# Optimization experiments

Hardware: AMD Instinct MI355X
Metric: run time of the kernel (lower is better)

The kernel has to match this reference:

```python
import jax, jax.numpy as jnp
import numpy as np

B, C, H, W = 16, 512, 25, 25
HEADS = 8
HID = 2048
PATCH = 5  # hardcoded patch_size in FusionAttention
EPS_LN = 1e-5
EPS_BN = 1e-5


def _channel_layernorm(x, g, b):
    # torch: std = var(unbiased=False).sqrt(); (x-mean)/(std+eps)*g + b, over channel dim=1
    mean = jnp.mean(x, axis=1, keepdims=True)
    var = jnp.var(x, axis=1, keepdims=True)
    return (x - mean) / (jnp.sqrt(var) + EPS_LN) * g + b


def _dwconv3x3(x, w, b):
    # depthwise 3x3, padding 1; w: (C,1,3,3)
    y = jax.lax.conv_general_dilated(
        x, w, window_strides=(1, 1), padding=((1, 1), (1, 1)),
        feature_group_count=x.shape[1],
        dimension_numbers=('NCHW', 'OIHW', 'NCHW'))
    return y + b[None, :, None, None]


def setup_inputs() -> dict:
    key = jax.random.key(0)
    ks = jax.random.split(key, 20)
    s = 0.02
    d = {
        'x': jax.random.normal(ks[0], (B, C, H, W), jnp.float32),
        'ln1_g': jnp.ones((1, C, 1, 1), jnp.float32),
        'ln1_b': jnp.zeros((1, C, 1, 1), jnp.float32),
        'wq': jax.random.normal(ks[1], (C, 1, 3, 3), jnp.float32) * s,
        'bq': jnp.zeros((C,), jnp.float32),
        'wk': jax.random.normal(ks[2], (C, 1, 3, 3), jnp.float32) * s,
        'bk': jnp.zeros((C,), jnp.float32),
        'wv': jax.random.normal(ks[3], (C, 1, 3, 3), jnp.float32) * s,
        'bv': jnp.zeros((C,), jnp.float32),
        'swq': jax.random.normal(ks[4], (C, 1, 3, 3), jnp.float32) * s,
        'sbq': jnp.zeros((C,), jnp.float32),
        'swk': jax.random.normal(ks[5], (C, 1, 3, 3), jnp.float32) * s,
        'sbk': jnp.zeros((C,), jnp.float32),
        'swv': jax.random.normal(ks[6], (C, 1, 3, 3), jnp.float32) * s,
        'sbv': jnp.zeros((C,), jnp.float32),
        'proj_w': jax.random.normal(ks[7], (C, C, 1, 1), jnp.float32) * s,
        'bn_g': jnp.ones((C,), jnp.float32),
        'bn_b': jnp.zeros((C,), jnp.float32),
        'bn_mean': jnp.zeros((C,), jnp.float32),
        'bn_var': jnp.ones((C,), jnp.float32),
        'ln2_g': jnp.ones((1, C, 1, 1), jnp.float32),
        'ln2_b': jnp.zeros((1, C, 1, 1), jnp.float32),
        'w1': jax.random.normal(ks[8], (HID, C, 1, 1), jnp.float32) * s,
        'b1': jnp.zeros((HID,), jnp.float32),
        'w2': jax.random.normal(ks[9], (C, HID, 1, 1), jnp.float32) * s,
        'b2': jnp.zeros((C,), jnp.float32),
    }
    return d


def _fusion_attention(x, wq, bq, wk, bk, wv, bv, swq, sbq, swk, sbk, swv, sbv,
                      proj_w, bn_g, bn_b, bn_mean, bn_var):
    b, c, h, w = x.shape
    n = h * w
    hd = c // HEADS
    scale = hd ** -0.5

    def split_heads(t):  # (b,c,h,w) -> (b, heads, n, hd)
        return t.reshape(b, HEADS, hd, n).transpose(0, 1, 3, 2)

    q = split_heads(_dwconv3x3(x, wq, bq))
    k = split_heads(_dwconv3x3(x, wk, bk))
    v = split_heads(_dwconv3x3(x, wv, bv))

    dots = jnp.einsum('bhid,bhjd->bhij', q, k) * scale
    attn = jax.nn.softmax(dots, axis=-1)
    out = jnp.einsum('bhij,bhjd->bhid', attn, v)
    # rearrange 'b h (H W) d -> b (h d) H W' with H=PATCH
    out = out.transpose(0, 1, 3, 2).reshape(b, c, PATCH, n // PATCH)

    spe_q = _dwconv3x3(out, swq, sbq).reshape(b, c, n)          # b d (l w)
    spe_k = _dwconv3x3(out, swk, sbk).reshape(b, c, n).transpose(0, 2, 1)  # b (l w) d
    spe_v = _dwconv3x3(out, swv, sbv).reshape(b, c, n)

    attention = jax.nn.softmax(jnp.einsum('bcn,bnd->bcd', spe_q, spe_k) * scale, axis=-1)
    x_out = jnp.einsum('bcd,bdn->bcn', attention, spe_v).reshape(b, c, h, w)

    # 1x1 conv (no bias) + BatchNorm2d (eval mode)
    proj = jnp.einsum('oc,bchw->bohw', proj_w[:, :, 0, 0], x_out)
    proj = (proj - bn_mean[None, :, None, None]) / jnp.sqrt(bn_var + EPS_BN)[None, :, None, None]
    proj = proj * bn_g[None, :, None, None] + bn_b[None, :, None, None]
    return proj


def _feedforward(x, w1, b1, w2, b2):
    h1 = jnp.einsum('oc,bchw->bohw', w1[:, :, 0, 0], x) + b1[None, :, None, None]
    h1 = jax.nn.gelu(h1, approximate=False)
    return jnp.einsum('oc,bchw->bohw', w2[:, :, 0, 0], h1) + b2[None, :, None, None]


def reference(x, ln1_g, ln1_b, wq, bq, wk, bk, wv, bv, swq, sbq, swk, sbk,
              swv, sbv, proj_w, bn_g, bn_b, bn_mean, bn_var, ln2_g, ln2_b,
              w1, b1, w2, b2):
    y1 = x + _fusion_attention(_channel_layernorm(x, ln1_g, ln1_b),
                               wq, bq, wk, bk, wv, bv, swq, sbq, swk, sbk,
                               swv, sbv, proj_w, bn_g, bn_b, bn_mean, bn_var)
    y_out = y1 + _feedforward(_channel_layernorm(y1, ln2_g, ln2_b), w1, b1, w2, b2)
    return y_out
```

## Files before the change

kernel.cpp:

```cpp
#include <hip/hip_runtime.h>
#include <math.h>

constexpr int BATCH = 16;
constexpr int CH    = 512;
constexpr int NPIX  = 625;
constexpr int HEADS = 8;
constexpr int HDIM  = 64;
constexpr int HIDD  = 2048;

constexpr float EPS_LN = 1e-5f;
constexpr float EPS_BN = 1e-5f;
constexpr float SCALE  = 0.125f;

typedef __bf16 bf16x8 __attribute__((ext_vector_type(8)));
typedef float  f32x4  __attribute__((ext_vector_type(4)));

static __device__ inline unsigned pack_bf16(float lo, float hi) {
  union { __bf16 h; unsigned short u; } a, b;
  a.h = (__bf16)lo; b.h = (__bf16)hi;
  return ((unsigned)b.u << 16) | (unsigned)a.u;
}

__global__ __launch_bounds__(256) void ln_kernel2(
    const float* __restrict__ x, const float* __restrict__ g,
    const float* __restrict__ bt, float* __restrict__ y) {
  __shared__ float ps[4][64];
  __shared__ float pss[4][64];
  int lane = threadIdx.x & 63;
  int w    = threadIdx.x >> 6;
  int b    = blockIdx.y;
  int i    = blockIdx.x * 64 + lane;
  int ic   = i < NPIX ? i : NPIX - 1;
  const float* xb = x + (size_t)b * CH * NPIX + ic;
  float s = 0.f, ss = 0.f;
  #pragma unroll 4
  for (int c = w * 128; c < w * 128 + 128; ++c) {
    float v = xb[(size_t)c * NPIX];
    s += v; ss += v * v;
  }
  ps[w][lane] = s; pss[w][lane] = ss;
  __syncthreads();
  float st  = ps[0][lane] + ps[1][lane] + ps[2][lane] + ps[3][lane];
  float sst = pss[0][lane] + pss[1][lane] + pss[2][lane] + pss[3][lane];
  float mean = st * (1.0f / CH);
  float var  = sst * (1.0f / CH) - mean * mean;
  float inv  = 1.0f / (sqrtf(fmaxf(var, 0.0f)) + EPS_LN);
  if (i >= NPIX) return;
  float* yb = y + (size_t)b * CH * NPIX + i;
  #pragma unroll 4
  for (int c = w * 128; c < w * 128 + 128; ++c) {
    float v = xb[(size_t)c * NPIX];
    yb[(size_t)c * NPIX] = (v - mean) * inv * g[c] + bt[c];
  }
}

__global__ void dwconv3_kernel(const float* __restrict__ src,
    const float* __restrict__ w0, const float* __restrict__ b0,
    const float* __restrict__ w1, const float* __restrict__ b1,
    const float* __restrict__ w2, const float* __restrict__ b2,
    float* __restrict__ d0, float* __restrict__ d1, float* __restrict__ d2,
    int Hc, int Wc) {
  size_t idx = (size_t)blockIdx.x * blockDim.x + threadIdx.x;
  size_t total = (size_t)BATCH * CH * Hc * Wc;
  if (idx >= total) return;
  int wp = (int)(idx % Wc);
  int hp = (int)((idx / Wc) % Hc);
  int c  = (int)((idx / ((size_t)Wc * Hc)) % CH);
  const float* f0 = w0 + c * 9;
  const float* f1 = w1 + c * 9;
  const float* f2 = w2 + c * 9;
  float a0 = 0.f, a1 = 0.f, a2 = 0.f;
  #pragma unroll
  for (int kh = -1; kh <= 1; ++kh) {
    int h2 = hp + kh; if (h2 < 0 || h2 >= Hc) continue;
    #pragma unroll
    for (int kw = -1; kw <= 1; ++kw) {
      int w2p = wp + kw; if (w2p < 0 || w2p >= Wc) continue;
      float v = src[idx + (size_t)kh * Wc + kw];
      int wi = (kh + 1) * 3 + (kw + 1);
      a0 += v * f0[wi]; a1 += v * f1[wi]; a2 += v * f2[wi];
    }
  }
  d0[idx] = a0 + b0[c];
  d1[idx] = a1 + b1[c];
  d2[idx] = a2 + b2[c];
}

__global__ void dwconv_spe_kernel(const float* __restrict__ src,
    const float* __restrict__ w0, const float* __restrict__ b0,
    const float* __restrict__ w1, const float* __restrict__ b1,
    const float* __restrict__ w2, const float* __restrict__ b2,
    __bf16* __restrict__ q16, __bf16* __restrict__ k16, float* __restrict__ v) {
  size_t idx = (size_t)blockIdx.x * blockDim.x + threadIdx.x;
  if (idx >= (size_t)BATCH * CH * 640) return;
  int n = (int)(idx % 640);
  int c = (int)((idx / 640) % CH);
  int b = (int)(idx / ((size_t)640 * CH));
  if (n >= NPIX) { q16[idx] = (__bf16)0.f; k16[idx] = (__bf16)0.f; return; }
  int hp = n / 125, wp = n % 125;
  size_t base = ((size_t)b * CH + c) * NPIX;
  const float* f0 = w0 + c * 9;
  const float* f1 = w1 + c * 9;
  const float* f2 = w2 + c * 9;
  float a0 = 0.f, a1 = 0.f, a2 = 0.f;
  #pragma unroll
  for (int kh = -1; kh <= 1; ++kh) {
    int h2 = hp + kh; if (h2 < 0 || h2 >= 5) continue;
    #pragma unroll
    for (int kw = -1; kw <= 1; ++kw) {
      int w2p = wp + kw; if (w2p < 0 || w2p >= 125) continue;
      float vv = src[base + h2 * 125 + w2p];
      int wi = (kh + 1) * 3 + (kw + 1);
      a0 += vv * f0[wi]; a1 += vv * f1[wi]; a2 += vv * f2[wi];
    }
  }
  q16[idx] = (__bf16)(a0 + b0[c]);
  k16[idx] = (__bf16)(a1 + b1[c]);
  v[base + n] = a2 + b2[c];
}

__global__ __launch_bounds__(256) void qk_to_bf16T(
    const float* __restrict__ q, const float* __restrict__ k,
    __bf16* __restrict__ qT, __bf16* __restrict__ kT) {
  __shared__ __bf16 tq[64][65];
  __shared__ __bf16 tk[64][65];
  int bh = blockIdx.y;
  int n0 = blockIdx.x * 64;
  int b = bh >> 3, h = bh & 7;
  const float* qb = q + (size_t)(b * CH + h * HDIM) * NPIX;
  const float* kb = k + (size_t)(b * CH + h * HDIM) * NPIX;
  #pragma unroll
  for (int it = 0; it < 16; ++it) {
    int idx = threadIdx.x + it * 256;
    int d = idx >> 6, n = idx & 63;
    int nn = n0 + n;
    float qv = (nn < NPIX) ? qb[(size_t)d * NPIX + nn] : 0.f;
    float kv = (nn < NPIX) ? kb[(size_t)d * NPIX + nn] : 0.f;
    tq[n][d] = (__bf16)qv;
    tk[n][d] = (__bf16)kv;
  }
  __syncthreads();
  size_t obase = (size_t)bh * NPIX;
  #pragma unroll
  for (int it = 0; it < 16; ++it) {
    int idx = threadIdx.x + it * 256;
    int n = idx >> 6, d = idx & 63;
    int nn = n0 + n;
    if (nn < NPIX) {
      qT[(obase + nn) * 64 + d] = tq[n][d];
      kT[(obase + nn) * 64 + d] = tk[n][d];
    }
  }
}

__global__ void v_to_bf16(const float* __restrict__ v, __bf16* __restrict__ v16) {
  int row = blockIdx.x;
  const float* src = v + (size_t)row * NPIX;
  __bf16* dst = v16 + (size_t)row * 640;
  for (int n = threadIdx.x; n < NPIX; n += 256) dst[n] = (__bf16)src[n];
}

__global__ __launch_bounds__(256) void head_attn_mfma4(
    const __bf16* __restrict__ qT, const __bf16* __restrict__ kT,
    const __bf16* __restrict__ vB, float* __restrict__ out) {
  __shared__ __align__(16) union SmU {
    unsigned char p[16 * 1296];
    float ostage[64][17];
  } sm;
  __shared__ float red_max[4][16];
  __shared__ float red_sum[4][16];

  int t = threadIdx.x;
  int w = t >> 6, lane = t & 63, g = lane >> 4, li = lane & 15;
  int h = blockIdx.y, b = blockIdx.z;
  int bh = b * HEADS + h;
  int i0 = blockIdx.x * 16;
  const __bf16* Qb = qT + (size_t)bh * NPIX * 64;
  const __bf16* Kb = kT + (size_t)bh * NPIX * 64;

  bf16x8 aq0, aq1;
  {
    int qr = i0 + li; if (qr > NPIX - 1) qr = NPIX - 1;
    const __bf16* qp = Qb + (size_t)qr * 64 + 8 * g;
    aq0 = *(const bf16x8*)(qp);
    aq1 = *(const bf16x8*)(qp + 32);
  }

  f32x4 s[10];
  #pragma unroll
  for (int cfl = 0; cfl < 10; ++cfl) {
    int kc = (w * 10 + cfl) * 16 + li;
    int kcl = kc > NPIX - 1 ? NPIX - 1 : kc;
    const __bf16* kp = Kb + (size_t)kcl * 64 + 8 * g;
    bf16x8 bk0 = *(const bf16x8*)(kp);
    bf16x8 bk1 = *(const bf16x8*)(kp + 32);
    f32x4 a = (f32x4){0.f, 0.f, 0.f, 0.f};
    a = __builtin_amdgcn_mfma_f32_16x16x32_bf16(aq0, bk0, a, 0, 0, 0);
    a = __builtin_amdgcn_mfma_f32_16x16x32_bf16(aq1, bk1, a, 0, 0, 0);
    s[cfl] = a * SCALE;
  }
  if (w == 3 && li > 0) {
    s[9][0] = -1e30f; s[9][1] = -1e30f; s[9][2] = -1e30f; s[9][3] = -1e30f;
  }

  #pragma unroll
  for (int r = 0; r < 4; ++r) {
    float mx = s[0][r];
    #pragma unroll
    for (int cfl = 1; cfl < 10; ++cfl) mx = fmaxf(mx, s[cfl][r]);
    mx = fmaxf(mx, __shfl_xor(mx, 1));
    mx = fmaxf(mx, __shfl_xor(mx, 2));
    mx = fmaxf(mx, __shfl_xor(mx, 4));
    mx = fmaxf(mx, __shfl_xor(mx, 8));
    if (li == 0) red_max[w][4 * g + r] = mx;
  }
  __syncthreads();

  #pragma unroll
  for (int r = 0; r < 4; ++r) {
    int row = 4 * g + r;
    float mx = fmaxf(fmaxf(red_max[0][row], red_max[1][row]),
                     fmaxf(red_max[2][row], red_max[3][row]));
    float sum = 0.f;
    #pragma unroll
    for (int cfl = 0; cfl < 10; ++cfl) {
      float p = __expf(s[cfl][r] - mx);
      s[cfl][r] = p;
      sum += p;
    }
    sum += __shfl_xor(sum, 1);
    sum += __shfl_xor(sum, 2);
    sum += __shfl_xor(sum, 4);
    sum += __shfl_xor(sum, 8);
    if (li == 0) red_sum[w][row] = sum;
  }
  __syncthreads();

  #pragma unroll
  for (int cfp = 0; cfp < 5; ++cfp) {
    int cf0 = 2 * cfp, cf1 = cf0 + 1;
    #pragma unroll
    for (int r = 0; r < 4; ++r) {
      float v0 = s[cf0][r], v1 = s[cf1][r];
      float t0 = __shfl_xor(v0, 1);
      float t1 = __shfl_xor(v1, 1);
      bool even = (li & 1) == 0;
      float lo = even ? v0 : t1;
      float hi = even ? t0 : v1;
      int col = even ? ((w * 10 + cf0) * 16 + li)
                     : ((w * 10 + cf1) * 16 + li - 1);
      int row = 4 * g + r;
      *(unsigned*)(&sm.p[row * 1296 + col * 2]) = pack_bf16(lo, hi);
    }
  }
  __syncthreads();

  const __bf16* vrow = vB + (size_t)(b * CH + h * HDIM + w * 16 + li) * 640;
  f32x4 oa = (f32x4){0.f, 0.f, 0.f, 0.f};
  f32x4 ob = (f32x4){0.f, 0.f, 0.f, 0.f};
  #pragma unroll
  for (int ks = 0; ks < 20; ks += 2) {
    bf16x8 pa0 = *(const bf16x8*)(&sm.p[li * 1296 + ks * 64 + 16 * g]);
    bf16x8 bv0 = *(const bf16x8*)(vrow + ks * 32 + 8 * g);
    oa = __builtin_amdgcn_mfma_f32_16x16x32_bf16(pa0, bv0, oa, 0, 0, 0);
    bf16x8 pa1 = *(const bf16x8*)(&sm.p[li * 1296 + (ks + 1) * 64 + 16 * g]);
    bf16x8 bv1 = *(const bf16x8*)(vrow + (ks + 1) * 32 + 8 * g);
    ob = __builtin_amdgcn_mfma_f32_16x16x32_bf16(pa1, bv1, ob, 0, 0, 0);
  }
  f32x4 o = oa + ob;
  #pragma unroll
  for (int r = 0; r < 4; ++r) {
    int row = 4 * g + r;
    float l = red_sum[0][row] + red_sum[1][row] + red_sum[2][row] + red_sum[3][row];
    o[r] *= (1.0f / l);
  }
  __syncthreads();

  #pragma unroll
  for (int r = 0; r < 4; ++r)
    sm.ostage[w * 16 + li][4 * g + r] = o[r];
  __syncthreads();
  size_t cbase = (size_t)(b * CH + h * HDIM);
  #pragma unroll
  for (int it = 0; it < 4; ++it) {
    int e = t + it * 256;
    int d = e >> 4, nl = e & 15;
    int n = i0 + nl;
    if (n < NPIX) out[(cbase + d) * NPIX + n] = sm.ostage[d][nl];
  }
}

__global__ __launch_bounds__(256) void chan_attn_mfma2(
    const __bf16* __restrict__ sq, const __bf16* __restrict__ sk,
    __bf16* __restrict__ Am) {
  __shared__ float red_max[4][16];
  __shared__ float red_sum[4][16];
  int t = threadIdx.x;
  int w = t >> 6, lane = t & 63, g = lane >> 4, li = lane & 15;
  int b = blockIdx.y;
  int cq0 = blockIdx.x * 16;
  const __bf16* qrow  = sq + ((size_t)b * CH + cq0 + li) * 640 + 8 * g;
  const __bf16* kbase = sk + ((size_t)b * CH + w * 128 + li) * 640 + 8 * g;
  f32x4 acc[8];
  #pragma unroll
  for (int i = 0; i < 8; ++i) acc[i] = (f32x4){0.f, 0.f, 0.f, 0.f};
  for (int ks = 0; ks < 20; ++ks) {
    bf16x8 af = *(const bf16x8*)(qrow + ks * 32);
    #pragma unroll
    for (int cfl = 0; cfl < 8; ++cfl) {
      bf16x8 bfr = *(const bf16x8*)(kbase + (size_t)cfl * 16 * 640 + ks * 32);
      acc[cfl] = __builtin_amdgcn_mfma_f32_16x16x32_bf16(af, bfr, acc[cfl], 0, 0, 0);
    }
  }
  #pragma unroll
  for (int i = 0; i < 8; ++i) acc[i] = acc[i] * SCALE;

  #pragma unroll
  for (int r = 0; r < 4; ++r) {
    float mx = acc[0][r];
    #pragma unroll
    for (int cfl = 1; cfl < 8; ++cfl) mx = fmaxf(mx, acc[cfl][r]);
    mx = fmaxf(mx, __shfl_xor(mx, 1));
    mx = fmaxf(mx, __shfl_xor(mx, 2));
    mx = fmaxf(mx, __shfl_xor(mx, 4));
    mx = fmaxf(mx, __shfl_xor(mx, 8));
    if (li == 0) red_max[w][4 * g + r] = mx;
  }
  __syncthreads();

  #pragma unroll
  for (int r = 0; r < 4; ++r) {
    int row = 4 * g + r;
    float mx = fmaxf(fmaxf(red_max[0][row], red_max[1][row]),
                     fmaxf(red_max[2][row], red_max[3][row]));
    float sum = 0.f;
    #pragma unroll
    for (int cfl = 0; cfl < 8; ++cfl) {
      float p = __expf(acc[cfl][r] - mx);
      acc[cfl][r] = p;
      sum += p;
    }
    sum += __shfl_xor(sum, 1);
    sum += __shfl_xor(sum, 2);
    sum += __shfl_xor(sum, 4);
    sum += __shfl_xor(sum, 8);
    if (li == 0) red_sum[w][row] = sum;
  }
  __syncthreads();

  __bf16* Ab = Am + ((size_t)b * CH + cq0) * CH + w * 128;
  #pragma unroll
  for (int r = 0; r < 4; ++r) {
    int row = 4 * g + r;
    float l = red_sum[0][row] + red_sum[1][row] + red_sum[2][row] + red_sum[3][row];
    float inv = 1.0f / l;
    #pragma unroll
    for (int cfl = 0; cfl < 8; ++cfl)
      Ab[(size_t)row * CH + cfl * 16 + li] = (__bf16)(acc[cfl][r] * inv);
  }
}

template <int EPI>
__global__ __launch_bounds__(256) void gemm_nt(
    const __bf16* __restrict__ A, long long aBatch,
    const __bf16* __restrict__ B, long long bBatch,
    void* __restrict__ Cout, long long cBatch,
    int M, int N, int K,
    const float* __restrict__ p0, const float* __restrict__ p1,
    const float* __restrict__ res, long long resBatch) {
  __shared__ __align__(16) union {
    struct { unsigned char As[128 * 128]; unsigned char Bs[64 * 128]; } s;
    float Ce[4][64][17];
  } u;
  int t = threadIdx.x;
  int w = t >> 6, lane = t & 63, g = lane >> 4, li = lane & 15;
  int wm = w & 1, wn = w >> 1;
  int n0 = blockIdx.x * 64, m0 = blockIdx.y * 128, b = blockIdx.z;
  const __bf16* Ab = A + (size_t)b * aBatch;
  const __bf16* Bb = B + (size_t)b * bBatch;
  f32x4 acc[4][2];
  #pragma unroll
  for (int i = 0; i < 4; ++i)
    #pragma unroll
    for (int j = 0; j < 2; ++j) acc[i][j] = (f32x4){0.f, 0.f, 0.f, 0.f};

  for (int k0 = 0; k0 < K; k0 += 64) {
    bf16x8 ra[4], rb[2];
    #pragma unroll
    for (int i = 0; i < 4; ++i) {
      int e = t + i * 256;
      int row = e >> 3, cc = e & 7;
      int ar = m0 + row; ar = ar < M ? ar : M - 1;
      ra[i] = *(const bf16x8*)(Ab + (size_t)ar * K + k0 + cc * 8);
    }
    #pragma unroll
    for (int i = 0; i < 2; ++i) {
      int e = t + i * 256;
      int row = e >> 3, cc = e & 7;
      rb[i] = *(const bf16x8*)(Bb + (size_t)(n0 + row) * K + k0 + cc * 8);
    }
    __syncthreads();
    #pragma unroll
    for (int i = 0; i < 4; ++i) {
      int e = t + i * 256; int row = e >> 3, cc = e & 7;
      int off = (row * 128 + cc * 16) ^ ((row & 7) << 4);
      *(bf16x8*)(&u.s.As[off]) = ra[i];
    }
    #pragma unroll
    for (int i = 0; i < 2; ++i) {
      int e = t + i * 256; int row = e >> 3, cc = e & 7;
      int off = (row * 128 + cc * 16) ^ ((row & 7) << 4);
      *(bf16x8*)(&u.s.Bs[off]) = rb[i];
    }
    __syncthreads();
    #pragma unroll
    for (int ks = 0; ks < 2; ++ks) {
      bf16x8 af[4], bfr[2];
      #pragma unroll
      for (int mf = 0; mf < 4; ++mf) {
        int row = wm * 64 + mf * 16 + li;
        int off = (row * 128 + ks * 64 + g * 16) ^ ((row & 7) << 4);
        af[mf] = *(const bf16x8*)(&u.s.As[off]);
      }
      #pragma unroll
      for (int nf = 0; nf < 2; ++nf) {
        int row = wn * 32 + nf * 16 + li;
        int off = (row * 128 + ks * 64 + g * 16) ^ ((row & 7) << 4);
        bfr[nf] = *(const bf16x8*)(&u.s.Bs[off]);
      }
      #pragma unroll
      for (int mf = 0; mf < 4; ++mf)
        #pragma unroll
        for (int nf = 0; nf < 2; ++nf)
          acc[mf][nf] = __builtin_amdgcn_mfma_f32_16x16x32_bf16(
              af[mf], bfr[nf], acc[mf][nf], 0, 0, 0);
    }
    __syncthreads();
  }

  #pragma unroll
  for (int p = 0; p < 2; ++p) {
    __syncthreads();
    #pragma unroll
    for (int mf = 0; mf < 4; ++mf) {
      #pragma unroll
      for (int r = 0; r < 4; ++r)
        u.Ce[w][mf * 16 + 4 * g + r][li] = acc[mf][p][r];
    }
    __syncthreads();
    int m = m0 + wm * 64 + lane;
    int colb = n0 + wn * 32 + p * 16;
    if (m < M) {
      float vv[16];
      #pragma unroll
      for (int c = 0; c < 16; ++c) vv[c] = u.Ce[w][lane][c];
      if (EPI == 0) {
        __bf16* Cb = (__bf16*)Cout + (size_t)b * cBatch + (size_t)m * N + colb;
        bf16x8 o0, o1;
        #pragma unroll
        for (int j = 0; j < 8; ++j) { o0[j] = (__bf16)vv[j]; o1[j] = (__bf16)vv[8 + j]; }
        *(bf16x8*)(Cb) = o0;
        *(bf16x8*)(Cb + 8) = o1;
      } else if (EPI == 1) {
        float* Cf = (float*)Cout + (size_t)b * cBatch + (size_t)m * N + colb;
        const float* rp = res + (size_t)b * resBatch + (size_t)m * N + colb;
        #pragma unroll
        for (int c = 0; c < 16; ++c)
          vv[c] = vv[c] * p0[colb + c] + p1[colb + c] + rp[c];
        #pragma unroll
        for (int c4 = 0; c4 < 4; ++c4)
          *(f32x4*)(Cf + c4 * 4) = (f32x4){vv[c4*4], vv[c4*4+1], vv[c4*4+2], vv[c4*4+3]};
      } else if (EPI == 2) {
        __bf16* Cb = (__bf16*)Cout + (size_t)b * cBatch + (size_t)m * N + colb;
        #pragma unroll
        for (int c = 0; c < 16; ++c) {
          float xg = vv[c] + p0[colb + c];
          vv[c] = 0.5f * xg * (1.0f + erff(xg * 0.70710678118654752f));
        }
        bf16x8 o0, o1;
        #pragma unroll
        for (int j = 0; j < 8; ++j) { o0[j] = (__bf16)vv[j]; o1[j] = (__bf16)vv[8 + j]; }
        *(bf16x8*)(Cb) = o0;
        *(bf16x8*)(Cb + 8) = o1;
      } else {
        float* Cf = (float*)Cout + (size_t)b * cBatch + (size_t)m * N + colb;
        const float* rp = res + (size_t)b * resBatch + (size_t)m * N + colb;
        #pragma unroll
        for (int c = 0; c < 16; ++c)
          vv[c] = vv[c] + p0[colb + c] + rp[c];
        #pragma unroll
        for (int c4 = 0; c4 < 4; ++c4)
          *(f32x4*)(Cf + c4 * 4) = (f32x4){vv[c4*4], vv[c4*4+1], vv[c4*4+2], vv[c4*4+3]};
      }
    }
  }
}

template <typename TO>
__global__ __launch_bounds__(256) void transpose_bat(
    const float* __restrict__ in, TO* __restrict__ out, int R, int Cc) {
  __shared__ float tile[64][65];
  int b = blockIdx.z;
  int c0 = blockIdx.x * 64, r0 = blockIdx.y * 64;
  const float* ib = in + (size_t)b * R * Cc;
  TO* ob = out + (size_t)b * R * Cc;
  for (int e = threadIdx.x; e < 4096; e += 256) {
    int rr = e >> 6, cc = e & 63;
    int r = r0 + rr, c = c0 + cc;
    tile[rr][cc] = (r < R && c < Cc) ? ib[(size_t)r * Cc + c] : 0.f;
  }
  __syncthreads();
  for (int e = threadIdx.x; e < 4096; e += 256) {
    int cc = e >> 6, rr = e & 63;
    int r = r0 + rr, c = c0 + cc;
    if (r < R && c < Cc) ob[(size_t)c * R + r] = (TO)tile[rr][cc];
  }
}

__global__ __launch_bounds__(256) void ln2_row_kernel(
    const float* __restrict__ y, const float* __restrict__ g,
    const float* __restrict__ bt, __bf16* __restrict__ o) {
  int row = blockIdx.x * 4 + (threadIdx.x >> 6);
  int lane = threadIdx.x & 63;
  const float* yr = y + (size_t)row * CH + lane * 8;
  f32x4 v0 = *(const f32x4*)(yr);
  f32x4 v1 = *(const f32x4*)(yr + 4);
  float s = v0[0]+v0[1]+v0[2]+v0[3]+v1[0]+v1[1]+v1[2]+v1[3];
  float ss = v0[0]*v0[0]+v0[1]*v0[1]+v0[2]*v0[2]+v0[3]*v0[3]
           + v1[0]*v1[0]+v1[1]*v1[1]+v1[2]*v1[2]+v1[3]*v1[3];
  #pragma unroll
  for (int off = 32; off > 0; off >>= 1) {
    s  += __shfl_xor(s, off);
    ss += __shfl_xor(ss, off);
  }
  float mean = s * (1.0f / CH);
  float var  = ss * (1.0f / CH) - mean * mean;
  float inv  = 1.0f / (sqrtf(fmaxf(var, 0.0f)) + EPS_LN);
  f32x4 g0 = *(const f32x4*)(g + lane * 8);
  f32x4 g1 = *(const f32x4*)(g + lane * 8 + 4);
  f32x4 b0 = *(const f32x4*)(bt + lane * 8);
  f32x4 b1 = *(const f32x4*)(bt + lane * 8 + 4);
  bf16x8 ov;
  #pragma unroll
  for (int j = 0; j < 4; ++j) ov[j]     = (__bf16)((v0[j] - mean) * inv * g0[j] + b0[j]);
  #pragma unroll
  for (int j = 0; j < 4; ++j) ov[4 + j] = (__bf16)((v1[j] - mean) * inv * g1[j] + b1[j]);
  *(bf16x8*)(o + (size_t)row * CH + lane * 8) = ov;
}

__global__ void cast_bf16_kernel(const float* __restrict__ s, __bf16* __restrict__ d, int n) {
  int i = blockIdx.x * 256 + threadIdx.x;
  if (i < n) d[i] = (__bf16)s[i];
}

__global__ void bn_prep(const float* __restrict__ g, const float* __restrict__ bt,
                        const float* __restrict__ mean, const float* __restrict__ var,
                        float* __restrict__ scale, float* __restrict__ shift) {
  int c = blockIdx.x * blockDim.x + threadIdx.x;
  if (c >= CH) return;
  float s = g[c] * rsqrtf(var[c] + EPS_BN);
  scale[c] = s;
  shift[c] = bt[c] - mean[c] * s;
}

extern "C" void kernel_launch(void* const* d_in, const int* in_sizes, int n_in,
                              void* d_out, int out_size, void* d_ws, size_t ws_size,
                              hipStream_t stream) {
  const float* x      = (const float*)d_in[0];
  const float* ln1_g  = (const float*)d_in[1];
  const float* ln1_b  = (const float*)d_in[2];
  const float* wq     = (const float*)d_in[3];
  const float* bq     = (const float*)d_in[4];
  const float* wk     = (const float*)d_in[5];
  const float* bk     = (const float*)d_in[6];
  const float* wv     = (const float*)d_in[7];
  const float* bv     = (const float*)d_in[8];
  const float* swq    = (const float*)d_in[9];
  const float* sbq    = (const float*)d_in[10];
  const float* swk    = (const float*)d_in[11];
  const float* sbk    = (const float*)d_in[12];
  const float* swv    = (const float*)d_in[13];
  const float* sbv    = (const float*)d_in[14];
  const float* proj_w = (const float*)d_in[15];
  const float* bn_g   = (const float*)d_in[16];
  const float* bn_b   = (const float*)d_in[17];
  const float* bn_m   = (const float*)d_in[18];
  const float* bn_v   = (const float*)d_in[19];
  const float* ln2_g  = (const float*)d_in[20];
  const float* ln2_b  = (const float*)d_in[21];
  const float* w1     = (const float*)d_in[22];
  const float* b1     = (const float*)d_in[23];
  const float* w2     = (const float*)d_in[24];
  const float* b2     = (const float*)d_in[25];

  char* W = (char*)d_ws;
  const size_t SZB = 20480000;
  char* S0 = W;
  char* S1 = W + SZB;
  char* S2 = W + 2 * SZB;
  char* S3 = W + 3 * SZB;
  char* S4 = W + 4 * SZB;

  float*  xln   = (float*)S0;
  float*  qb    = (float*)S1;
  float*  kb    = (float*)S2;
  float*  vb    = (float*)S3;
  __bf16* qT    = (__bf16*)S0;
  __bf16* kTp   = qT + (size_t)BATCH * HEADS * NPIX * 64;
  __bf16* v16   = (__bf16*)d_out;
  float*  ab    = (float*)S4;
  __bf16* sq16  = (__bf16*)S1;
  __bf16* sk16  = (__bf16*)S2;
  float*  sv    = (float*)S3;
  __bf16* svT   = (__bf16*)S4;
  __bf16* Amat  = (__bf16*)S0;
  __bf16* pw16  = (__bf16*)(S0 + 10485760);
  __bf16* w116  = (__bf16*)(S0 + 10485760 + 524288);
  __bf16* w216  = (__bf16*)(S0 + 10485760 + 524288 + 2097152);
  float*  bnsc  = (float*)(S0 + 10485760 + 524288 + 2097152 + 2097152);
  float*  bnsh  = bnsc + CH;
  __bf16* xoutT = (__bf16*)S1;
  float*  x_nc  = (float*)S4;
  float*  y1_nc = (float*)S3;
  __bf16* y1ln  = (__bf16*)S0;
  __bf16* h1T   = (__bf16*)S1;
  float*  tmp_nc = (float*)S4;

  const size_t SZ = (size_t)BATCH * CH * NPIX;

  ln_kernel2<<<dim3(10, BATCH), 256, 0, stream>>>(x, ln1_g, ln1_b, xln);
  dwconv3_kernel<<<(int)((SZ + 255) / 256), 256, 0, stream>>>(
      xln, wq, bq, wk, bk, wv, bv, qb, kb, vb, 25, 25);
  qk_to_bf16T<<<dim3(10, BATCH * HEADS), 256, 0, stream>>>(qb, kb, qT, kTp);
  v_to_bf16<<<dim3(BATCH * CH), 256, 0, stream>>>(vb, v16);
  head_attn_mfma4<<<dim3(40, HEADS, BATCH), 256, 0, stream>>>(qT, kTp, v16, ab);
  dwconv_spe_kernel<<<(int)(((size_t)BATCH * CH * 640 + 255) / 256), 256, 0, stream>>>(
      ab, swq, sbq, swk, sbk, swv, sbv, sq16, sk16, sv);
  transpose_bat<__bf16><<<dim3(10, 8, BATCH), 256, 0, stream>>>(sv, svT, CH, NPIX);
  cast_bf16_kernel<<<1024, 256, 0, stream>>>(proj_w, pw16, CH * CH);
  cast_bf16_kernel<<<4096, 256, 0, stream>>>(w1, w116, HIDD * CH);
  cast_bf16_kernel<<<4096, 256, 0, stream>>>(w2, w216, CH * HIDD);
  bn_prep<<<2, 256, 0, stream>>>(bn_g, bn_b, bn_m, bn_v, bnsc, bnsh);
  chan_attn_mfma2<<<dim3(32, BATCH), 256, 0, stream>>>(sq16, sk16, Amat);
  gemm_nt<0><<<dim3(8, 5, BATCH), 256, 0, stream>>>(
      svT, (long long)NPIX * CH, Amat, (long long)CH * CH,
      xoutT, (long long)NPIX * CH, NPIX, CH, CH,
      nullptr, nullptr, nullptr, 0);
  transpose_bat<float><<<dim3(10, 8, BATCH), 256, 0, stream>>>(x, x_nc, CH, NPIX);
  gemm_nt<1><<<dim3(8, 79, 1), 256, 0, stream>>>(
      xoutT, 0LL, pw16, 0LL, y1_nc, 0LL, BATCH * NPIX, CH, CH,
      bnsc, bnsh, x_nc, 0LL);
  ln2_row_kernel<<<BATCH * NPIX / 4, 256, 0, stream>>>(y1_nc, ln2_g, ln2_b, y1ln);
  gemm_nt<2><<<dim3(32, 79, 1), 256, 0, stream>>>(
      y1ln, 0LL, w116, 0LL, h1T, 0LL, BATCH * NPIX, HIDD, CH,
      b1, nullptr, nullptr, 0LL);
  gemm_nt<3><<<dim3(8, 79, 1), 256, 0, stream>>>(
      h1T, 0LL, w216, 0LL, tmp_nc, 0LL, BATCH * NPIX, CH, HIDD,
      b2, nullptr, y1_nc, 0LL);
  transpose_bat<float><<<dim3(8, 10, BATCH), 256, 0, stream>>>(
      tmp_nc, (float*)d_out, NPIX, CH);
}
```

Baseline: 582.6 us.

## Rewrite head attention: wave-per-query-tile, register-resident probabilities, no max pass

The head attention kernel now gives each wave 16 query rows across all keys, and each block covers 64 queries. Grid blocks drop from 40 to 10 per head. The key operand feeds the MFMA A side, so probabilities come out key-major. They are exponentiated, packed to bf16 in registers, and rearranged with lane shuffles into the A operand of the PV MFMA, replacing the LDS round-trip and the cross-wave max/sum reductions with their barriers. The softmax max subtraction is dropped, which removes a reduction pass but risks overflow if attention scores grow large. It also raises register pressure by holding 40 packed probability tiles per lane.

```diff
diff --git a/kernel.cpp b/kernel.cpp
--- a/kernel.cpp
+++ b/kernel.cpp
@@ -14,6 +14,7 @@
 
 typedef __bf16 bf16x8 __attribute__((ext_vector_type(8)));
 typedef float  f32x4  __attribute__((ext_vector_type(4)));
+typedef unsigned u32x4 __attribute__((ext_vector_type(4)));
 
 static __device__ inline unsigned pack_bf16(float lo, float hi) {
   union { __bf16 h; unsigned short u; } a, b;
@@ -160,133 +161,99 @@
   for (int n = threadIdx.x; n < NPIX; n += 256) dst[n] = (__bf16)src[n];
 }
 
-__global__ __launch_bounds__(256) void head_attn_mfma4(
+__global__ __launch_bounds__(256) void head_attn_mfma5(
     const __bf16* __restrict__ qT, const __bf16* __restrict__ kT,
     const __bf16* __restrict__ vB, float* __restrict__ out) {
-  __shared__ __align__(16) union SmU {
-    unsigned char p[16 * 1296];
-    float ostage[64][17];
-  } sm;
-  __shared__ float red_max[4][16];
-  __shared__ float red_sum[4][16];
-
+  __shared__ float lds_o[64][68];
   int t = threadIdx.x;
   int w = t >> 6, lane = t & 63, g = lane >> 4, li = lane & 15;
   int h = blockIdx.y, b = blockIdx.z;
   int bh = b * HEADS + h;
-  int i0 = blockIdx.x * 16;
+  int i0 = blockIdx.x * 64;
+  int qr0 = i0 + w * 16;
   const __bf16* Qb = qT + (size_t)bh * NPIX * 64;
   const __bf16* Kb = kT + (size_t)bh * NPIX * 64;
 
-  bf16x8 aq0, aq1;
+  bf16x8 bq0, bq1;
   {
-    int qr = i0 + li; if (qr > NPIX - 1) qr = NPIX - 1;
+    int qr = qr0 + li; if (qr > NPIX - 1) qr = NPIX - 1;
     const __bf16* qp = Qb + (size_t)qr * 64 + 8 * g;
-    aq0 = *(const bf16x8*)(qp);
-    aq1 = *(const bf16x8*)(qp + 32);
-  }
-
-  f32x4 s[10];
-  #pragma unroll
-  for (int cfl = 0; cfl < 10; ++cfl) {
-    int kc = (w * 10 + cfl) * 16 + li;
-    int kcl = kc > NPIX - 1 ? NPIX - 1 : kc;
-    const __bf16* kp = Kb + (size_t)kcl * 64 + 8 * g;
-    bf16x8 bk0 = *(const bf16x8*)(kp);
-    bf16x8 bk1 = *(const bf16x8*)(kp + 32);
+    bq0 = *(const bf16x8*)(qp);
+    bq1 = *(const bf16x8*)(qp + 32);
+  }
+
+  uint2 pv[40];
+  float suml = 0.f;
+  #pragma unroll
+  for (int cf = 0; cf < 40; ++cf) {
+    int kr = cf * 16 + li; if (kr > NPIX - 1) kr = NPIX - 1;
+    const __bf16* kp = Kb + (size_t)kr * 64 + 8 * g;
+    bf16x8 ak0 = *(const bf16x8*)(kp);
+    bf16x8 ak1 = *(const bf16x8*)(kp + 32);
     f32x4 a = (f32x4){0.f, 0.f, 0.f, 0.f};
-    a = __builtin_amdgcn_mfma_f32_16x16x32_bf16(aq0, bk0, a, 0, 0, 0);
-    a = __builtin_amdgcn_mfma_f32_16x16x32_bf16(aq1, bk1, a, 0, 0, 0);
-    s[cfl] = a * SCALE;
-  }
-  if (w == 3 && li > 0) {
-    s[9][0] = -1e30f; s[9][1] = -1e30f; s[9][2] = -1e30f; s[9][3] = -1e30f;
-  }
-
-  #pragma unroll
-  for (int r = 0; r < 4; ++r) {
-    float mx = s[0][r];
-    #pragma unroll
-    for (int cfl = 1; cfl < 10; ++cfl) mx = fmaxf(mx, s[cfl][r]);
-    mx = fmaxf(mx, __shfl_xor(mx, 1));
-    mx = fmaxf(mx, __shfl_xor(mx, 2));
-    mx = fmaxf(mx, __shfl_xor(mx, 4));
-    mx = fmaxf(mx, __shfl_xor(mx, 8));
-    if (li == 0) red_max[w][4 * g + r] = mx;
-  }
-  __syncthreads();
-
-  #pragma unroll
-  for (int r = 0; r < 4; ++r) {
-    int row = 4 * g + r;
-    float mx = fmaxf(fmaxf(red_max[0][row], red_max[1][row]),
-                     fmaxf(red_max[2][row], red_max[3][row]));
-    float sum = 0.f;
-    #pragma unroll
-    for (int cfl = 0; cfl < 10; ++cfl) {
-      float p = __expf(s[cfl][r] - mx);
-      s[cfl][r] = p;
-      sum += p;
-    }
-    sum += __shfl_xor(sum, 1);
-    sum += __shfl_xor(sum, 2);
-    sum += __shfl_xor(sum, 4);
-    sum += __shfl_xor(sum, 8);
-    if (li == 0) red_sum[w][row] = sum;
-  }
-  __syncthreads();
-
-  #pragma unroll
-  for (int cfp = 0; cfp < 5; ++cfp) {
-    int cf0 = 2 * cfp, cf1 = cf0 + 1;
-    #pragma unroll
-    for (int r = 0; r < 4; ++r) {
-      float v0 = s[cf0][r], v1 = s[cf1][r];
-      float t0 = __shfl_xor(v0, 1);
-      float t1 = __shfl_xor(v1, 1);
-      bool even = (li & 1) == 0;
-      float lo = even ? v0 : t1;
-      float hi = even ? t0 : v1;
-      int col = even ? ((w * 10 + cf0) * 16 + li)
-                     : ((w * 10 + cf1) * 16 + li - 1);
-      int row = 4 * g + r;
-      *(unsigned*)(&sm.p[row * 1296 + col * 2]) = pack_bf16(lo, hi);
-    }
-  }
-  __syncthreads();
-
-  const __bf16* vrow = vB + (size_t)(b * CH + h * HDIM + w * 16 + li) * 640;
-  f32x4 oa = (f32x4){0.f, 0.f, 0.f, 0.f};
-  f32x4 ob = (f32x4){0.f, 0.f, 0.f, 0.f};
-  #pragma unroll
-  for (int ks = 0; ks < 20; ks += 2) {
-    bf16x8 pa0 = *(const bf16x8*)(&sm.p[li * 1296 + ks * 64 + 16 * g]);
-    bf16x8 bv0 = *(const bf16x8*)(vrow + ks * 32 + 8 * g);
-    oa = __builtin_amdgcn_mfma_f32_16x16x32_bf16(pa0, bv0, oa, 0, 0, 0);
-    bf16x8 pa1 = *(const bf16x8*)(&sm.p[li * 1296 + (ks + 1) * 64 + 16 * g]);
-    bf16x8 bv1 = *(const bf16x8*)(vrow + (ks + 1) * 32 + 8 * g);
-    ob = __builtin_amdgcn_mfma_f32_16x16x32_bf16(pa1, bv1, ob, 0, 0, 0);
-  }
-  f32x4 o = oa + ob;
-  #pragma unroll
-  for (int r = 0; r < 4; ++r) {
-    int row = 4 * g + r;
-    float l = red_sum[0][row] + red_sum[1][row] + red_sum[2][row] + red_sum[3][row];
-    o[r] *= (1.0f / l);
-  }
-  __syncthreads();
-
-  #pragma unroll
-  for (int r = 0; r < 4; ++r)
-    sm.ostage[w * 16 + li][4 * g + r] = o[r];
+    a = __builtin_amdgcn_mfma_f32_16x16x32_bf16(ak0, bq0, a, 0, 0, 0);
+    a = __builtin_amdgcn_mfma_f32_16x16x32_bf16(ak1, bq1, a, 0, 0, 0);
+    float e0 = __expf(a[0] * SCALE);
+    float e1 = __expf(a[1] * SCALE);
+    float e2 = __expf(a[2] * SCALE);
+    float e3 = __expf(a[3] * SCALE);
+    if (cf == 39) {
+      e1 = 0.f; e2 = 0.f; e3 = 0.f;
+      if (g > 0) e0 = 0.f;
+    }
+    suml += e0 + e1 + e2 + e3;
+    pv[cf].x = pack_bf16(e0, e1);
+    pv[cf].y = pack_bf16(e2, e3);
+  }
+  suml += __shfl_xor(suml, 16);
+  suml += __shfl_xor(suml, 32);
+  float inv = 1.0f / suml;
+  float invr[4];
+  #pragma unroll
+  for (int r = 0; r < 4; ++r) invr[r] = __shfl(inv, 4 * g + r);
+
+  const __bf16* Vb = vB + (size_t)(b * CH + h * HDIM) * 640;
+  f32x4 o[4];
+  #pragma unroll
+  for (int dg = 0; dg < 4; ++dg) o[dg] = (f32x4){0.f, 0.f, 0.f, 0.f};
+  int L0 = ((2 * g) & 3) * 16 + li;
+  int L1 = L0 + 16;
+  bool hi = (g >= 2);
+  #pragma unroll
+  for (int ks = 0; ks < 20; ++ks) {
+    int xA0 = (int)pv[2 * ks].x,     xA1 = (int)pv[2 * ks].y;
+    int xB0 = (int)pv[2 * ks + 1].x, xB1 = (int)pv[2 * ks + 1].y;
+    int a0A = __shfl(xA0, L0), a0B = __shfl(xB0, L0);
+    int a1A = __shfl(xA1, L0), a1B = __shfl(xB1, L0);
+    int a2A = __shfl(xA0, L1), a2B = __shfl(xB0, L1);
+    int a3A = __shfl(xA1, L1), a3B = __shfl(xB1, L1);
+    u32x4 aw;
+    aw[0] = (unsigned)(hi ? a0B : a0A);
+    aw[1] = (unsigned)(hi ? a1B : a1A);
+    aw[2] = (unsigned)(hi ? a2B : a2A);
+    aw[3] = (unsigned)(hi ? a3B : a3A);
+    bf16x8 pa = __builtin_bit_cast(bf16x8, aw);
+    #pragma unroll
+    for (int dg = 0; dg < 4; ++dg) {
+      bf16x8 bv = *(const bf16x8*)(Vb + (size_t)(dg * 16 + li) * 640 + ks * 32 + 8 * g);
+      o[dg] = __builtin_amdgcn_mfma_f32_16x16x32_bf16(pa, bv, o[dg], 0, 0, 0);
+    }
+  }
+
+  #pragma unroll
+  for (int dg = 0; dg < 4; ++dg) {
+    #pragma unroll
+    for (int r = 0; r < 4; ++r)
+      lds_o[w * 16 + 4 * g + r][dg * 16 + li] = o[dg][r] * invr[r];
+  }
   __syncthreads();
   size_t cbase = (size_t)(b * CH + h * HDIM);
-  #pragma unroll
-  for (int it = 0; it < 4; ++it) {
+  int qmax = NPIX - i0;
+  #pragma unroll
+  for (int it = 0; it < 16; ++it) {
     int e = t + it * 256;
-    int d = e >> 4, nl = e & 15;
-    int n = i0 + nl;
-    if (n < NPIX) out[(cbase + d) * NPIX + n] = sm.ostage[d][nl];
+    int q = e & 63, d = e >> 6;
+    if (q < qmax) out[(cbase + d) * NPIX + i0 + q] = lds_o[q][d];
   }
 }
 
@@ -633,7 +600,7 @@
       xln, wq, bq, wk, bk, wv, bv, qb, kb, vb, 25, 25);
   qk_to_bf16T<<<dim3(10, BATCH * HEADS), 256, 0, stream>>>(qb, kb, qT, kTp);
   v_to_bf16<<<dim3(BATCH * CH), 256, 0, stream>>>(vb, v16);
-  head_attn_mfma4<<<dim3(40, HEADS, BATCH), 256, 0, stream>>>(qT, kTp, v16, ab);
+  head_attn_mfma5<<<dim3(10, HEADS, BATCH), 256, 0, stream>>>(qT, kTp, v16, ab);
   dwconv_spe_kernel<<<(int)(((size_t)BATCH * CH * 640 + 255) / 256), 256, 0, stream>>>(
       ab, swq, sbq, swk, sbk, swv, sbv, sq16, sk16, sv);
   transpose_bat<__bf16><<<dim3(10, 8, BATCH), 256, 0, stream>>>(sv, svT, CH, NPIX);
```

Result: slower. 595.3 us (+2.2%).
